# Kernel optimization log

Measured on AMD Instinct MI355X. Metric: run time of the kernel, lower is better.

Reference implementation:

```python
import jax, jax.numpy as jnp
import numpy as np

GROUP = 32  # hadamard_group_size == MXFP4 block size
FP4_GRID = np.array([0.0, 0.5, 1.0, 1.5, 2.0, 3.0, 4.0, 6.0], dtype=np.float32)  # e2m1 magnitudes
FP4_MID = np.array([0.25, 0.75, 1.25, 1.75, 2.5, 3.5, 5.0], dtype=np.float32)    # RTN midpoints


def _hadamard(n):
    # Sylvester construction, normalized so H is orthonormal (matches hadamard(n)*n**-0.5)
    H = np.array([[1.0]], dtype=np.float64)
    while H.shape[0] < n:
        H = np.block([[H, H], [H, -H]])
    return (H / np.sqrt(n)).astype(np.float32)


def _pseudo_quant_mxfp4(t, H, gs):
    """Hadamard-rotate per group of 32, then MXFP4 (e2m1 + power-of-two block scale)
    quant-dequant with abs_max scaling and a global scale. STE through the rounding."""
    shp = t.shape
    rot = t.reshape(-1, GROUP) @ H                      # [n_groups, 32] rotated space
    v = jax.lax.stop_gradient(rot) * gs
    absmax = jnp.max(jnp.abs(v), axis=-1, keepdims=True)
    # E8M0 power-of-two shared scale so that absmax/scale <= 6 (max e2m1 value)
    scale = jnp.exp2(jnp.ceil(jnp.log2(absmax / 6.0 + 1e-30)))
    scale = jnp.where(absmax > 0, scale, 1.0)
    u = v / scale
    grid = jnp.asarray(FP4_GRID)
    mid = jnp.asarray(FP4_MID)
    q = jnp.sign(u) * grid[jnp.searchsorted(mid, jnp.abs(u))]  # round-to-nearest e2m1
    dq = q * scale / gs
    out = rot + jax.lax.stop_gradient(dq - rot)         # straight-through estimator
    return out.reshape(shp)


def setup_inputs() -> dict:
    key = jax.random.key(0)
    kx, kw, kb = jax.random.split(key, 3)
    B, S, K, N = 4, 2048, 4096, 4096
    x = jax.random.normal(kx, (B, S, K), jnp.float32)
    weight = jax.random.normal(kw, (N, K), jnp.float32) * (K ** -0.5)
    bias = jax.random.normal(kb, (N,), jnp.float32)
    H = jnp.asarray(_hadamard(GROUP))
    weight_global_scale = jnp.array([3.0], jnp.float32)  # abs_max method
    act_global_scale = jnp.array([3.0], jnp.float32)
    return {"x": x, "weight": weight, "bias": bias, "hadamard_matrix": H,
            "weight_global_scale": weight_global_scale, "act_global_scale": act_global_scale}


def reference(x, weight, bias, hadamard_matrix, weight_global_scale, act_global_scale):
    x_dq = _pseudo_quant_mxfp4(x, hadamard_matrix, act_global_scale[0])
    w_dq = _pseudo_quant_mxfp4(weight, hadamard_matrix, weight_global_scale[0])
    # both operands stay in the rotated space; per-group Hadamard is orthogonal so
    # x_rot @ w_rot^T == x @ w^T up to quantization error (QuTLASS semantics)
    return jnp.einsum('bsk,nk->bsn', x_dq, w_dq) + bias
```

## Files before the change

kernel.cpp:

```cpp
#include <hip/hip_runtime.h>
#include <hip/hip_bf16.h>

typedef int   i32x4  __attribute__((ext_vector_type(4)));
typedef int   i32x8  __attribute__((ext_vector_type(8)));
typedef float f32x16 __attribute__((ext_vector_type(16)));

__device__ inline void gload_lds16(const void* g, void* l) {
  __builtin_amdgcn_global_load_lds((const __attribute__((address_space(1))) void*)g,
                                   (__attribute__((address_space(3))) void*)l, 16, 0, 0);
}
__device__ inline void gload_lds4(const void* g, void* l) {
  __builtin_amdgcn_global_load_lds((const __attribute__((address_space(1))) void*)g,
                                   (__attribute__((address_space(3))) void*)l, 4, 0, 0);
}
__device__ inline i32x8 pad8(i32x4 v) {
  i32x8 r;
  r[0] = v[0]; r[1] = v[1]; r[2] = v[2]; r[3] = v[3];
  r[4] = 0; r[5] = 0; r[6] = 0; r[7] = 0;
  return r;
}

__global__ __launch_bounds__(256) void quant_fused(const float* __restrict__ x,
                                                   const float* __restrict__ wt,
                                                   unsigned char* __restrict__ xq,
                                                   unsigned char* __restrict__ xsc,
                                                   unsigned char* __restrict__ wq,
                                                   unsigned char* __restrict__ wsc,
                                                   const float* __restrict__ ags,
                                                   const float* __restrict__ wgs,
                                                   int xg, int Mrows, int Nrows, int kg) {
  const int first = blockIdx.x * 256;
  const bool isX = first < xg;
  const float* in        = isX ? x   : wt;
  unsigned char* outq    = isX ? xq  : wq;
  unsigned char* outsc   = isX ? xsc : wsc;
  const float gs         = isX ? ags[0] : wgs[0];
  const int rows         = isX ? Mrows : Nrows;
  const int base         = isX ? first : first - xg;
  const int g = base + threadIdx.x;
  const int r = g / kg, j = g - r * kg;

  float t[32];
  const float4* p4 = (const float4*)(in + (size_t)g * 32);
#pragma unroll
  for (int i = 0; i < 8; ++i) {
    float4 v4 = p4[i];
    t[4 * i + 0] = v4.x; t[4 * i + 1] = v4.y;
    t[4 * i + 2] = v4.z; t[4 * i + 3] = v4.w;
  }
#pragma unroll
  for (int s = 0; s < 5; ++s) {
    const int hh = 1 << s;
#pragma unroll
    for (int i = 0; i < 32; ++i) {
      if ((i & hh) == 0) {
        float a = t[i], b = t[i + hh];
        t[i] = a + b;
        t[i + hh] = a - b;
      }
    }
  }

  const float c = 0.17677669529663687f;
  float v[32];
  float am = 0.0f;
#pragma unroll
  for (int i = 0; i < 32; ++i) {
    float vi = (t[i] * c) * gs;
    v[i] = vi;
    am = fmaxf(am, fabsf(vi));
  }

  float a6 = am / 6.0f;
  int ex;
  float mant = frexpf(a6, &ex);
  int e = (mant == 0.5f) ? ex - 1 : ex;
  if (e < -127) e = -127;
  if (e > 127) e = 127;
  float inv_s = ldexpf(1.0f, -e);

  unsigned int dw[4] = {0u, 0u, 0u, 0u};
#pragma unroll
  for (int i = 0; i < 32; ++i) {
    float u = v[i] * inv_s;
    float au = fabsf(u);
    int idx = (au > 0.25f) + (au > 0.75f) + (au > 1.25f) + (au > 1.75f)
            + (au > 2.5f) + (au > 3.5f) + (au > 5.0f);
    int code = idx | ((u < 0.0f) ? 8 : 0);
    dw[i >> 3] |= (unsigned)code << ((i & 7) * 4);
  }
  i32x4 packed;
  packed[0] = (int)dw[0]; packed[1] = (int)dw[1];
  packed[2] = (int)dw[2]; packed[3] = (int)dw[3];
  *(i32x4*)(outq + (size_t)r * ((size_t)kg * 16) + (size_t)j * 16) = packed;

  int s = j >> 3, j0 = j & 7;
  int p = ((j0 & 1) << 2) | (j0 >> 1);
  if (kg == 128) {
    __shared__ unsigned char sl[256];
    sl[(s << 4) | ((r & 1) << 3) | p] = (unsigned char)(e + 127);
    __syncthreads();
    if (threadIdx.x < 64) {
      int si = threadIdx.x >> 2, wd = threadIdx.x & 3;
      unsigned int vv = *(const unsigned int*)&sl[(si << 4) | (wd << 2)];
      size_t r0 = (size_t)(base / 128);
      *(unsigned int*)(outsc + ((size_t)si * rows + r0) * 8 + (wd << 2)) = vv;
    }
  } else {
    outsc[((size_t)s * rows + r) * 8 + p] = (unsigned char)(e + 127);
  }
}


#define STAGE(mb, kt, h, ldsHalf) do {                                               \
    const unsigned char* _s = (mb) + (size_t)((h)*64 + (w << 3) + (l >> 3)) * KB2    \
                      + (size_t)(kt) * 128 + (size_t)csw * 16;                       \
    gload_lds16(_s, (unsigned char*)(ldsHalf) + (w << 10));                          \
    gload_lds16(_s + ((size_t)KB2 << 5), (unsigned char*)(ldsHalf) + (w << 10) + 4096); \
  } while (0)

#define STAGE_ASC(kt, bf) gload_lds4(AscG + ((size_t)(kt) * M + brow) * 8 + (tid << 2), \
                                     (unsigned char*)&asc[bf][0] + (w << 8))
#define STAGE_BSC(kt, bf) gload_lds4(BscG + ((size_t)(kt) * N + bcol) * 8 + (tid << 2), \
                                     (unsigned char*)&bsc[bf][0] + (w << 8))

#define STAGESET(kt, bf) do {                                                        \
    STAGE(Ab, kt, 0, &lds[bf][0][0][0]); STAGE(Ab, kt, 1, &lds[bf][0][1][0]);        \
    STAGE_ASC(kt, bf);                                                               \
    STAGE(Bb, kt, 0, &lds[bf][1][0][0]); STAGE(Bb, kt, 1, &lds[bf][1][1][0]);        \
    STAGE_BSC(kt, bf);                                                               \
  } while (0)

#define READFRAGS(bf, AF, BF, SA, SB) do {                                           \
    const unsigned char* _bb = &lds[bf][1][0][0];                                    \
    _Pragma("unroll")                                                                \
    for (int nt = 0; nt < 2; ++nt) {                                                 \
      int row = wn * 64 + nt * 32 + (l & 31);                                        \
      int xr = row & 7;                                                              \
      _Pragma("unroll")                                                              \
      for (int kk = 0; kk < 4; ++kk)                                                 \
        BF[nt][kk] = *(const i32x4*)(_bb + row * 128 + (((kk * 2 + h) ^ xr) << 4));  \
      SB[nt] = *(const int*)((const unsigned char*)&bsc[bf][0] + row * 8 + h * 4);   \
    }                                                                                \
    const unsigned char* _ab = &lds[bf][0][0][0];                                    \
    _Pragma("unroll")                                                                \
    for (int mt = 0; mt < 2; ++mt) {                                                 \
      int row = wm * 64 + mt * 32 + (l & 31);                                        \
      int xr = row & 7;                                                              \
      _Pragma("unroll")                                                              \
      for (int kk = 0; kk < 4; ++kk)                                                 \
        AF[mt][kk] = *(const i32x4*)(_ab + row * 128 + (((kk * 2 + h) ^ xr) << 4));  \
      SA[mt] = *(const int*)((const unsigned char*)&asc[bf][0] + row * 8 + h * 4);   \
    }                                                                                \
  } while (0)

#define MF1(AF, BF, SA, SB, mt, nt, kk)                                              \
  acc[mt][nt] = __builtin_amdgcn_mfma_scale_f32_32x32x64_f8f6f4(                     \
      pad8(AF[mt][kk]), pad8(BF[nt][kk]), acc[mt][nt], 4, 4, kk, SA[mt], kk, SB[nt]);

#define MFMAQ_ALL(AF, BF, SA, SB) do {                                               \
    __builtin_amdgcn_s_setprio(1);                                                   \
    MF1(AF, BF, SA, SB, 0, 0, 0) MF1(AF, BF, SA, SB, 0, 1, 0)                        \
    MF1(AF, BF, SA, SB, 1, 0, 0) MF1(AF, BF, SA, SB, 1, 1, 0)                        \
    MF1(AF, BF, SA, SB, 0, 0, 1) MF1(AF, BF, SA, SB, 0, 1, 1)                        \
    MF1(AF, BF, SA, SB, 1, 0, 1) MF1(AF, BF, SA, SB, 1, 1, 1)                        \
    MF1(AF, BF, SA, SB, 0, 0, 2) MF1(AF, BF, SA, SB, 0, 1, 2)                        \
    MF1(AF, BF, SA, SB, 1, 0, 2) MF1(AF, BF, SA, SB, 1, 1, 2)                        \
    MF1(AF, BF, SA, SB, 0, 0, 3) MF1(AF, BF, SA, SB, 0, 1, 3)                        \
    MF1(AF, BF, SA, SB, 1, 0, 3) MF1(AF, BF, SA, SB, 1, 1, 3)                        \
    __builtin_amdgcn_s_setprio(0);                                                   \
  } while (0)

#define LGKM0() do { asm volatile("s_waitcnt lgkmcnt(0)" ::: "memory");              \
    __builtin_amdgcn_sched_barrier(0); } while (0)
#define VM6()  asm volatile("s_waitcnt vmcnt(6)" ::: "memory")

__global__ __launch_bounds__(256, 2) void gemm128_fp4(const unsigned char* __restrict__ Aq,
                                                      const unsigned char* __restrict__ Bq,
                                                      const unsigned char* __restrict__ AscG,
                                                      const unsigned char* __restrict__ BscG,
                                                      float* __restrict__ C,
                                                      const float* __restrict__ bias,
                                                      const float* __restrict__ gsx,
                                                      const float* __restrict__ gsw,
                                                      int M, int N, int K) {
  __shared__ __align__(16) unsigned char lds[2][2][2][8192];
  __shared__ __align__(16) unsigned char asc[2][1024];
  __shared__ __align__(16) unsigned char bsc[2][1024];

  const int tid = threadIdx.x;
  const int w = tid >> 6, l = tid & 63;
  const int wm = w >> 1, wn = w & 1;
  const int h = l >> 5;
  const int csw = (l & 7) ^ (l >> 3);
  const int KB2 = K >> 1;

  const int ntn = N >> 7;
  const int nwg = gridDim.x;
  int r_t, c_t;
  {
    int bid = blockIdx.x;
    if ((nwg & 7) == 0) {
      int x = bid & 7, o = bid >> 3, cpx = nwg >> 3;
      int rpx = cpx / ntn;
      if ((ntn & 7) == 0 && rpx > 0 && (cpx % ntn) == 0) {
        int g8 = o & 7, rr = (o >> 3) % rpx, ss = o / (8 * rpx);
        r_t = x * rpx + rr;
        c_t = ss * 8 + g8;
      } else {
        int lin = x * cpx + o;
        r_t = lin / ntn; c_t = lin % ntn;
      }
    } else {
      r_t = bid / ntn; c_t = bid % ntn;
    }
  }
  const size_t brow = (size_t)r_t * 128;
  const size_t bcol = (size_t)c_t * 128;

  const unsigned char* Ab = Aq + brow * (size_t)KB2;
  const unsigned char* Bb = Bq + bcol * (size_t)KB2;

  f32x16 acc[2][2];
#pragma unroll
  for (int m = 0; m < 2; ++m)
#pragma unroll
    for (int n = 0; n < 2; ++n)
#pragma unroll
      for (int r = 0; r < 16; ++r) acc[m][n][r] = 0.0f;

  i32x4 afA[2][4], bfrA[2][4];  int saA[2], sbA[2];
  i32x4 afB[2][4], bfrB[2][4];  int saB[2], sbB[2];

  const int nkt = K / 256;

  STAGESET(0, 0);
  STAGESET(1, 1);
  VM6();
  __builtin_amdgcn_s_barrier();
  READFRAGS(0, afA, bfrA, saA, sbA);
  LGKM0();
  __builtin_amdgcn_s_barrier();

  for (int t = 0; t < nkt; t += 2) {
    const int t2 = (t + 2 < nkt) ? t + 2 : nkt - 1;
    const int t3 = (t + 3 < nkt) ? t + 3 : nkt - 1;

    STAGESET(t2, 0);
    VM6();
    __builtin_amdgcn_s_barrier();
    READFRAGS(1, afB, bfrB, saB, sbB);
    MFMAQ_ALL(afA, bfrA, saA, sbA);
    LGKM0();
    __builtin_amdgcn_s_barrier();

    STAGESET(t3, 1);
    VM6();
    __builtin_amdgcn_s_barrier();
    READFRAGS(0, afA, bfrA, saA, sbA);
    MFMAQ_ALL(afB, bfrB, saB, sbB);
    LGKM0();
    __builtin_amdgcn_s_barrier();
  }

  const float inv = 1.0f / (gsx[0] * gsw[0]);
#pragma unroll
  for (int nt = 0; nt < 2; ++nt) {
    const int col = (int)bcol + wn * 64 + nt * 32 + (l & 31);
    const float bv = bias[col];
#pragma unroll
    for (int mt = 0; mt < 2; ++mt) {
      const size_t rbase = brow + (size_t)(wm * 64 + mt * 32 + 4 * h);
#pragma unroll
      for (int r = 0; r < 16; ++r) {
        const size_t row = rbase + (r & 3) + 8 * (r >> 2);
        C[row * (size_t)N + col] = acc[mt][nt][r] * inv + bv;
      }
    }
  }
}

extern "C" void kernel_launch(void* const* d_in, const int* in_sizes, int n_in,
                              void* d_out, int out_size, void* d_ws, size_t ws_size,
                              hipStream_t stream) {
  const float* x    = (const float*)d_in[0];
  const float* wgt  = (const float*)d_in[1];
  const float* bias = (const float*)d_in[2];
  const float* wgs  = (const float*)d_in[4];
  const float* ags  = (const float*)d_in[5];

  const int N = in_sizes[2];
  const int K = in_sizes[1] / N;
  const int M = in_sizes[0] / K;
  const int kg = K / 32;

  unsigned char* aq  = (unsigned char*)d_ws;
  unsigned char* bq  = aq + (size_t)M * (K / 2);
  unsigned char* asc = bq + (size_t)N * (K / 2);
  unsigned char* bsc = asc + (size_t)M * kg;

  const int xg = in_sizes[0] / 32;
  const int wg = in_sizes[1] / 32;
  quant_fused<<<dim3((xg + wg) / 256), dim3(256), 0, stream>>>(
      x, wgt, aq, asc, bq, bsc, ags, wgs, xg, M, N, kg);

  dim3 grid((M / 128) * (N / 128));
  gemm128_fp4<<<grid, dim3(256), 0, stream>>>(aq, bq, asc, bsc, (float*)d_out, bias,
                                              ags, wgs, M, N, K);
}
```

Measured before the change: 166.0 us.

## Restructure FP4 GEMM main loop to single-buffered fragments with in-place restaging

The GEMM main loop changes from a two-iteration unrolled ping-pong, where the next tile's fragments were read from LDS while the current tile's MFMAs ran, to one tile per iteration. Each iteration reads fragments from the current LDS buffer, drains LDS and hits a barrier, issues global-to-LDS loads for tile t+2 into that same buffer, then runs the MFMAs, with the vmcnt wait set to 10. This halves the fragment register sets, which cuts VGPR pressure, and B and its scales are now staged before A. The cost is that LDS reads no longer overlap MFMA execution, which adds exposed latency on every tile.

```diff
diff --git a/kernel.cpp b/kernel.cpp
--- a/kernel.cpp
+++ b/kernel.cpp
@@ -112,8 +112,8 @@
 }
 
 
-#define STAGE(mb, kt, h, ldsHalf) do {                                               \
-    const unsigned char* _s = (mb) + (size_t)((h)*64 + (w << 3) + (l >> 3)) * KB2    \
+#define STAGE(mb, kt, hh, ldsHalf) do {                                              \
+    const unsigned char* _s = (mb) + (size_t)((hh)*64 + (w << 3) + (l >> 3)) * KB2   \
                       + (size_t)(kt) * 128 + (size_t)csw * 16;                       \
     gload_lds16(_s, (unsigned char*)(ldsHalf) + (w << 10));                          \
     gload_lds16(_s + ((size_t)KB2 << 5), (unsigned char*)(ldsHalf) + (w << 10) + 4096); \
@@ -125,55 +125,57 @@
                                      (unsigned char*)&bsc[bf][0] + (w << 8))
 
 #define STAGESET(kt, bf) do {                                                        \
-    STAGE(Ab, kt, 0, &lds[bf][0][0][0]); STAGE(Ab, kt, 1, &lds[bf][0][1][0]);        \
+    STAGE(Bb, kt, 0, &lds[bf][1][0]); STAGE(Bb, kt, 1, &lds[bf][1][8192]);           \
+    STAGE_BSC(kt, bf);                                                               \
+    STAGE(Ab, kt, 0, &lds[bf][0][0]); STAGE(Ab, kt, 1, &lds[bf][0][8192]);           \
     STAGE_ASC(kt, bf);                                                               \
-    STAGE(Bb, kt, 0, &lds[bf][1][0][0]); STAGE(Bb, kt, 1, &lds[bf][1][1][0]);        \
-    STAGE_BSC(kt, bf);                                                               \
   } while (0)
 
-#define READFRAGS(bf, AF, BF, SA, SB) do {                                           \
-    const unsigned char* _bb = &lds[bf][1][0][0];                                    \
+#define LOADB(bf) do {                                                               \
+    const unsigned char* _bb = &lds[bf][1][0];                                       \
     _Pragma("unroll")                                                                \
     for (int nt = 0; nt < 2; ++nt) {                                                 \
       int row = wn * 64 + nt * 32 + (l & 31);                                        \
       int xr = row & 7;                                                              \
       _Pragma("unroll")                                                              \
       for (int kk = 0; kk < 4; ++kk)                                                 \
-        BF[nt][kk] = *(const i32x4*)(_bb + row * 128 + (((kk * 2 + h) ^ xr) << 4));  \
-      SB[nt] = *(const int*)((const unsigned char*)&bsc[bf][0] + row * 8 + h * 4);   \
-    }                                                                                \
-    const unsigned char* _ab = &lds[bf][0][0][0];                                    \
+        bfr[nt][kk] = *(const i32x4*)(_bb + row * 128 + (((kk * 2 + h) ^ xr) << 4)); \
+      sb[nt] = *(const int*)((const unsigned char*)&bsc[bf][0] + row * 8 + h * 4);   \
+    } } while (0)
+
+#define LOADA(bf) do {                                                               \
+    const unsigned char* _ab = &lds[bf][0][0];                                       \
     _Pragma("unroll")                                                                \
     for (int mt = 0; mt < 2; ++mt) {                                                 \
       int row = wm * 64 + mt * 32 + (l & 31);                                        \
       int xr = row & 7;                                                              \
       _Pragma("unroll")                                                              \
       for (int kk = 0; kk < 4; ++kk)                                                 \
-        AF[mt][kk] = *(const i32x4*)(_ab + row * 128 + (((kk * 2 + h) ^ xr) << 4));  \
-      SA[mt] = *(const int*)((const unsigned char*)&asc[bf][0] + row * 8 + h * 4);   \
-    }                                                                                \
-  } while (0)
-
-#define MF1(AF, BF, SA, SB, mt, nt, kk)                                              \
+        af[mt][kk] = *(const i32x4*)(_ab + row * 128 + (((kk * 2 + h) ^ xr) << 4));  \
+      sa[mt] = *(const int*)((const unsigned char*)&asc[bf][0] + row * 8 + h * 4);   \
+    } } while (0)
+
+#define MF1(mt, nt, kk)                                                              \
   acc[mt][nt] = __builtin_amdgcn_mfma_scale_f32_32x32x64_f8f6f4(                     \
-      pad8(AF[mt][kk]), pad8(BF[nt][kk]), acc[mt][nt], 4, 4, kk, SA[mt], kk, SB[nt]);
-
-#define MFMAQ_ALL(AF, BF, SA, SB) do {                                               \
+      pad8(af[mt][kk]), pad8(bfr[nt][kk]), acc[mt][nt], 4, 4, kk, sa[mt], kk, sb[nt]);
+
+#define MFMAQ16() do {                                                               \
     __builtin_amdgcn_s_setprio(1);                                                   \
-    MF1(AF, BF, SA, SB, 0, 0, 0) MF1(AF, BF, SA, SB, 0, 1, 0)                        \
-    MF1(AF, BF, SA, SB, 1, 0, 0) MF1(AF, BF, SA, SB, 1, 1, 0)                        \
-    MF1(AF, BF, SA, SB, 0, 0, 1) MF1(AF, BF, SA, SB, 0, 1, 1)                        \
-    MF1(AF, BF, SA, SB, 1, 0, 1) MF1(AF, BF, SA, SB, 1, 1, 1)                        \
-    MF1(AF, BF, SA, SB, 0, 0, 2) MF1(AF, BF, SA, SB, 0, 1, 2)                        \
-    MF1(AF, BF, SA, SB, 1, 0, 2) MF1(AF, BF, SA, SB, 1, 1, 2)                        \
-    MF1(AF, BF, SA, SB, 0, 0, 3) MF1(AF, BF, SA, SB, 0, 1, 3)                        \
-    MF1(AF, BF, SA, SB, 1, 0, 3) MF1(AF, BF, SA, SB, 1, 1, 3)                        \
+    MF1(0, 0, 0) MF1(0, 1, 0) MF1(1, 0, 0) MF1(1, 1, 0)                              \
+    MF1(0, 0, 1) MF1(0, 1, 1) MF1(1, 0, 1) MF1(1, 1, 1)                              \
+    MF1(0, 0, 2) MF1(0, 1, 2) MF1(1, 0, 2) MF1(1, 1, 2)                              \
+    MF1(0, 0, 3) MF1(0, 1, 3) MF1(1, 0, 3) MF1(1, 1, 3)                              \
     __builtin_amdgcn_s_setprio(0);                                                   \
   } while (0)
 
-#define LGKM0() do { asm volatile("s_waitcnt lgkmcnt(0)" ::: "memory");              \
-    __builtin_amdgcn_sched_barrier(0); } while (0)
-#define VM6()  asm volatile("s_waitcnt vmcnt(6)" ::: "memory")
+#define DRAIN_THEN_BAR() do {                                                        \
+    asm volatile("s_waitcnt lgkmcnt(0)" ::: "memory");                               \
+    __builtin_amdgcn_sched_barrier(0);                                               \
+    __builtin_amdgcn_s_barrier();                                                    \
+  } while (0)
+
+#define ENDP() __builtin_amdgcn_s_barrier()
+#define VM10() asm volatile("s_waitcnt vmcnt(10)" ::: "memory")
 
 __global__ __launch_bounds__(256, 2) void gemm128_fp4(const unsigned char* __restrict__ Aq,
                                                       const unsigned char* __restrict__ Bq,
@@ -184,7 +186,7 @@
                                                       const float* __restrict__ gsx,
                                                       const float* __restrict__ gsw,
                                                       int M, int N, int K) {
-  __shared__ __align__(16) unsigned char lds[2][2][2][8192];
+  __shared__ __align__(16) unsigned char lds[2][2][16384];
   __shared__ __align__(16) unsigned char asc[2][1024];
   __shared__ __align__(16) unsigned char bsc[2][1024];
 
@@ -229,38 +231,27 @@
 #pragma unroll
       for (int r = 0; r < 16; ++r) acc[m][n][r] = 0.0f;
 
-  i32x4 afA[2][4], bfrA[2][4];  int saA[2], sbA[2];
-  i32x4 afB[2][4], bfrB[2][4];  int saB[2], sbB[2];
+  i32x4 af[2][4], bfr[2][4];
+  int sa[2], sb[2];
 
   const int nkt = K / 256;
 
   STAGESET(0, 0);
   STAGESET(1, 1);
-  VM6();
+  VM10();
   __builtin_amdgcn_s_barrier();
-  READFRAGS(0, afA, bfrA, saA, sbA);
-  LGKM0();
-  __builtin_amdgcn_s_barrier();
-
-  for (int t = 0; t < nkt; t += 2) {
+
+  for (int t = 0; t < nkt; ++t) {
+    const int p = t & 1;
     const int t2 = (t + 2 < nkt) ? t + 2 : nkt - 1;
-    const int t3 = (t + 3 < nkt) ? t + 3 : nkt - 1;
-
-    STAGESET(t2, 0);
-    VM6();
-    __builtin_amdgcn_s_barrier();
-    READFRAGS(1, afB, bfrB, saB, sbB);
-    MFMAQ_ALL(afA, bfrA, saA, sbA);
-    LGKM0();
-    __builtin_amdgcn_s_barrier();
-
-    STAGESET(t3, 1);
-    VM6();
-    __builtin_amdgcn_s_barrier();
-    READFRAGS(0, afA, bfrA, saA, sbA);
-    MFMAQ_ALL(afB, bfrB, saB, sbB);
-    LGKM0();
-    __builtin_amdgcn_s_barrier();
+
+    LOADB(p); LOADA(p);
+    DRAIN_THEN_BAR();
+    STAGESET(t2, p);
+    __builtin_amdgcn_sched_barrier(0);
+    MFMAQ16();
+    VM10();
+    ENDP();
   }
 
   const float inv = 1.0f / (gsx[0] * gsw[0]);
```

New measurement: 148.7 us, median of 2. 1.12x faster.
